# Performance work log

Hardware: AMD Instinct MI355X
Metric: run time of the kernel (lower is better)

## Reference

```python
import jax, jax.numpy as jnp
import numpy as np

B = 4096
STATE_DIM = 64
OBS_DIM = 32
BASE_DEGREE = 8
TIME_STEPS = 96
EPS = 1e-7


def _degree(t):
    # get_degree: degree_params initialized to linspace(0,1,time_steps); used via .item() (static)
    p = float(t) / (TIME_STEPS - 1)
    scaled = 0.5 * (1.0 + np.sin(2.0 * np.pi * p))
    return BASE_DEGREE + int(2.0 * scaled)


def _cheby_fwd_and_jac(x, coeffs, degree):
    """ChebyKAN forward y[b,o] = sum_{i,d} coeffs[i,o,d] * cos(d*acos(clip(tanh(x[b,i]))))
    plus its analytic per-sample Jacobian J[b,o,i] (replaces the torch autograd loop)."""
    t_raw = jnp.tanh(x)                                   # [B, D]
    t_val = jnp.clip(t_raw, -1.0 + EPS, 1.0 - EPS)
    theta = jnp.arccos(t_val)                             # [B, D]
    dvals = jnp.arange(degree + 1, dtype=x.dtype)         # [deg+1]
    ang = theta[..., None] * dvals                        # [B, D, deg+1]
    cheb = jnp.cos(ang)
    ac = coeffs[..., : degree + 1]                        # [D, D, deg+1]
    y = jnp.einsum('bid,iod->bo', cheb, ac)               # [B, D]
    # d cheb / d x = d*sin(d*theta) * (1 - tanh(x)^2) * mask / sqrt(1 - t_val^2)
    mask = ((t_raw > -1.0 + EPS) & (t_raw < 1.0 - EPS)).astype(x.dtype)
    dtheta_dx = -(1.0 - t_raw * t_raw) * mask / jnp.sqrt(1.0 - t_val * t_val)  # [B, D]
    dcheb_dx = -dvals * jnp.sin(ang) * dtheta_dx[..., None]                    # [B, D, deg+1]
    jac = jnp.einsum('bid,iod->boi', dcheb_dx, ac)        # [B, D, D] = dY_o/dx_i
    return y, jac


def setup_inputs() -> dict:
    key = jax.random.key(0)
    ks = jax.random.split(key, 5)
    obs = jax.random.normal(ks[0], (B, OBS_DIM), jnp.float32)
    prev_state = jax.random.normal(ks[1], (B, STATE_DIM), jnp.float32)
    A = jax.random.normal(ks[2], (B, STATE_DIM, STATE_DIM), jnp.float32)
    prev_cov = A @ A.transpose(0, 2, 1) / STATE_DIM + jnp.eye(STATE_DIM, dtype=jnp.float32)  # SPD
    bound = 1.0 / np.sqrt(STATE_DIM * (BASE_DEGREE + 3))  # kaiming-uniform style
    coeffs = jax.random.uniform(ks[3], (STATE_DIM, STATE_DIM, BASE_DEGREE + 3), jnp.float32, -bound, bound)
    M = jax.random.normal(ks[4], (STATE_DIM, OBS_DIM), jnp.float32)
    q, _ = jnp.linalg.qr(M)                               # orthonormal columns
    obs_matrix = q.T.astype(jnp.float32)                  # [OBS_DIM, STATE_DIM], orthogonal rows
    log_Q_diag = jnp.zeros((STATE_DIM,), jnp.float32)
    log_R_diag = jnp.zeros((OBS_DIM,), jnp.float32)
    return dict(obs=obs, prev_state=prev_state, prev_cov=prev_cov, coeffs=coeffs,
                obs_matrix=obs_matrix, log_Q_diag=log_Q_diag, log_R_diag=log_R_diag, t=10)


def reference(obs, prev_state, prev_cov, coeffs, obs_matrix, log_Q_diag, log_R_diag, t):
    degree = _degree(t)
    state_pred, Fj = _cheby_fwd_and_jac(prev_state, coeffs, degree)   # [B,D], [B,D,D]
    q = jnp.exp(log_Q_diag)                                           # [D]
    r = jnp.exp(log_R_diag)                                           # [O]
    H = obs_matrix                                                    # [O, D]
    # cov_pred = F P F^T + Q
    cov_pred = jnp.einsum('bij,bjk,blk->bil', Fj, prev_cov, Fj) + jnp.diag(q)[None]
    obs_pred = state_pred @ H.T                                       # [B, O]
    residual = obs - obs_pred                                         # [B, O]
    # S = H Pp H^T + R
    S = jnp.einsum('ij,bjk,lk->bil', H, cov_pred, H) + jnp.diag(r)[None]
    S_inv = jnp.linalg.pinv(S)                                        # [B, O, O]
    PHt = jnp.einsum('bij,oj->bio', cov_pred, H)                      # [B, D, O]
    K = jnp.einsum('bio,bop->bip', PHt, S_inv)                        # [B, D, O]
    state_update = state_pred + jnp.einsum('bio,bo->bi', K, residual)
    I_KH = jnp.eye(STATE_DIM, dtype=cov_pred.dtype)[None] - jnp.einsum('bio,oj->bij', K, H)
    # Joseph form: (I-KH) Pp (I-KH)^T + K R K^T
    cov_update = (jnp.einsum('bij,bjk,blk->bil', I_KH, cov_pred, I_KH)
                  + jnp.einsum('bio,o,bjo->bij', K, r, K))
    cov_diag = jnp.diagonal(cov_update, axis1=1, axis2=2)
    return state_update, cov_update, cov_diag
```

## Files before the change

### kernel.cpp

```cpp
#include <hip/hip_runtime.h>
#include <math.h>


typedef float f4 __attribute__((ext_vector_type(4)));
typedef float f32x4 __attribute__((ext_vector_type(4)));
typedef short b16x8 __attribute__((ext_vector_type(8)));
typedef short b16x4 __attribute__((ext_vector_type(4)));
typedef unsigned int u32;
typedef unsigned int u32x4 __attribute__((ext_vector_type(4)));
typedef unsigned short u16;

#define EPSC 1e-7f
#define MFMA(a, b, c) __builtin_amdgcn_mfma_f32_16x16x32_bf16(a, b, c, 0, 0, 0)
static constexpr size_t CU_OFF = 4096 * 64;
static constexpr size_t CD_OFF = CU_OFF + 4096ull * 4096;

__device__ __forceinline__ void split2(float x, short &h, short &l) {
  u32 u = __float_as_uint(x);
  h = (short)(u >> 16);
  float rem = x - __uint_as_float(u & 0xffff0000u);
  l = (short)(__float_as_uint(rem) >> 16);
}
__device__ __forceinline__ u32 packsplit(float x) {
  u32 u = __float_as_uint(x) & 0xffff0000u;
  float rem = x - __uint_as_float(u);
  return u | (__float_as_uint(rem) >> 16);
}
__device__ __forceinline__ float unpackf(u32 v) {
  return __uint_as_float(v & 0xffff0000u) + __uint_as_float(v << 16);
}
union U8 { u32x4 u; b16x8 s; };
__device__ __forceinline__ void unpack8(u32x4 q0, u32x4 q1, b16x8 &hi,
                                        b16x8 &lo) {
  U8 H, L;
  H.u[0] = __builtin_amdgcn_perm(q0[1], q0[0], 0x07060302u);
  H.u[1] = __builtin_amdgcn_perm(q0[3], q0[2], 0x07060302u);
  H.u[2] = __builtin_amdgcn_perm(q1[1], q1[0], 0x07060302u);
  H.u[3] = __builtin_amdgcn_perm(q1[3], q1[2], 0x07060302u);
  L.u[0] = __builtin_amdgcn_perm(q0[1], q0[0], 0x05040100u);
  L.u[1] = __builtin_amdgcn_perm(q0[3], q0[2], 0x05040100u);
  L.u[2] = __builtin_amdgcn_perm(q1[1], q1[0], 0x05040100u);
  L.u[3] = __builtin_amdgcn_perm(q1[3], q1[2], 0x05040100u);
  hi = H.s;
  lo = L.s;
}
__device__ __forceinline__ void split8v(f4 a, f4 b, b16x8 &hi, b16x8 &lo) {
#pragma unroll
  for (int j = 0; j < 4; ++j) {
    short hh, ll;
    split2(a[j], hh, ll); hi[j] = hh; lo[j] = ll;
    split2(b[j], hh, ll); hi[4 + j] = hh; lo[4 + j] = ll;
  }
}

__global__ __launch_bounds__(256) void prep_kernel(
    const float *__restrict__ Hm, const float *__restrict__ logQ,
    const float *__restrict__ logR, void *__restrict__ ws) {
  u16 *Hh = (u16 *)ws;
  u16 *Hl = (u16 *)ws + 2048;
  float *wq = (float *)((char *)ws + 8192);
  float *wr = wq + 64;
  const int tid = (int)threadIdx.x;
  f4 a = *(const f4 *)(Hm + tid * 8);
  f4 b = *(const f4 *)(Hm + tid * 8 + 4);
  b16x8 hi, lo;
  split8v(a, b, hi, lo);
  *(b16x8 *)(Hh + tid * 8) = hi;
  *(b16x8 *)(Hl + tid * 8) = lo;
  if (tid < 64) wq[tid] = expf(logQ[tid]);
  else if (tid < 96) wr[tid - 64] = expf(logR[tid - 64]);
}

__global__ __launch_bounds__(256, 4) void kalman_fused(
    const float *__restrict__ obs, const float *__restrict__ prev_state,
    const float *__restrict__ prev_cov, const float *__restrict__ coeffs,
    const float *__restrict__ Hm, const int *__restrict__ tptr,
    const void *__restrict__ ws, float *__restrict__ out) {
  __shared__ __align__(16) unsigned char pool[40704];
  u16 *sPh = (u16 *)(pool);
  u16 *sPl = (u16 *)(pool + 8192);
  u32 *sT = (u32 *)(pool);
  u32 *sPHt = (u32 *)(pool);
  u32 *sK = (u32 *)(pool + 8192);
  u16 *sFh = (u16 *)(pool + 16384);
  u16 *sFl = (u16 *)(pool + 24576);
  u32 *sCov = (u32 *)(pool + 16384);
  float *ypart = (float *)(pool + 32768);
  float *sS = (float *)(pool + 32768);
  float *sChT = (float *)(pool + 33792);
  float *sDcT = (float *)(pool + 36864);
  float *sy = (float *)(pool + 39936);
  float *sresid = (float *)(pool + 40192);
  float *sq = (float *)(pool + 40320);
  float *sr = (float *)(pool + 40576);

  const u16 *wHh = (const u16 *)ws;
  const u16 *wHl = (const u16 *)ws + 2048;
  const float *wq = (const float *)((const char *)ws + 8192);
  const float *wr = wq + 64;

  const int tid = (int)threadIdx.x;
  const int b = (int)blockIdx.x;
  const int w = tid >> 6;
  const int l = tid & 63;
  const int lr = l & 15;
  const int h = l >> 4;

  const int tval = tptr[0];
  const float ang = 6.28318530717958647f * ((float)tval / 95.0f);
  const int D = 9 + (int)(1.0f + sinf(ang));

  {
    const float *Pg = prev_cov + (size_t)b * 4096;
#pragma unroll
    for (int e = 0; e < 4; ++e) {
      const int idx = tid + 256 * e;
      f4 v = *(const f4 *)(Pg + 4 * idx);
      const int r = idx >> 4, c = (idx & 15) * 4;
      const int x = (r & 7) << 3;
      b16x4 h4, l4;
#pragma unroll
      for (int j = 0; j < 4; ++j) {
        short hh, ll;
        split2(v[j], hh, ll);
        h4[j] = hh; l4[j] = ll;
      }
      *(b16x4 *)(sPh + r * 64 + (c ^ x)) = h4;
      *(b16x4 *)(sPl + r * 64 + (c ^ x)) = l4;
    }
    if (tid < 64) {
      sq[tid] = wq[tid];
      const float xx = prev_state[b * 64 + tid];
      const float tr_ = tanhf(xx);
      const float tv = fminf(fmaxf(tr_, -1.0f + EPSC), 1.0f - EPSC);
      const float sn = sqrtf(fmaxf(1.0f - tv * tv, 0.0f));
      const float mask = (tr_ > -1.0f + EPSC && tr_ < 1.0f - EPSC) ? 1.0f : 0.0f;
      const float dth = -(1.0f - tr_ * tr_) * mask / sn;
      float *ct = sChT + tid * 12;
      float *dt = sDcT + tid * 12;
      ct[0] = 1.f; ct[1] = tv; ct[11] = 0.f;
      dt[0] = 0.f; dt[1] = -dth * sn; dt[11] = 0.f;
      float cm2 = 1.f, cm1 = tv, sm2 = 0.f, sm1 = sn;
      const float tv2 = 2.f * tv;
#pragma unroll
      for (int d = 2; d <= 10; ++d) {
        const float cc = fmaf(tv2, cm1, -cm2);
        const float ss = fmaf(tv2, sm1, -sm2);
        ct[d] = (d < D) ? cc : 0.f;
        dt[d] = (d < D) ? (-dth * (float)d * ss) : 0.f;
        cm2 = cm1; cm1 = cc; sm2 = sm1; sm1 = ss;
      }
    } else if (tid < 96) {
      sr[tid - 64] = wr[tid - 64];
    }
  }
  __syncthreads();

  {
    const int o = tid & 63, g = tid >> 6;
    float yacc = 0.f;
    float fr[16];
#pragma unroll
    for (int ii = 0; ii < 16; ++ii) {
      const int i = g * 16 + ii;
      const float *cp = coeffs + (size_t)(i * 64 + o) * 11;
      f4 q0 = *(const f4 *)(cp);
      f4 q1 = *(const f4 *)(cp + 4);
      f4 q2 = *(const f4 *)(cp + 7);
      const float *ct = sChT + i * 12;
      const float *dt = sDcT + i * 12;
      f4 c0 = *(const f4 *)(ct), c1 = *(const f4 *)(ct + 4),
         c2 = *(const f4 *)(ct + 8);
      f4 e0 = *(const f4 *)(dt), e1 = *(const f4 *)(dt + 4),
         e2 = *(const f4 *)(dt + 8);
      float yac = q0[0];
      yac = fmaf(q0[1], c0[1], yac);
      yac = fmaf(q0[2], c0[2], yac);
      yac = fmaf(q0[3], c0[3], yac);
      yac = fmaf(q1[0], c1[0], yac);
      yac = fmaf(q1[1], c1[1], yac);
      yac = fmaf(q1[2], c1[2], yac);
      yac = fmaf(q1[3], c1[3], yac);
      yac = fmaf(q2[1], c2[0], yac);
      yac = fmaf(q2[2], c2[1], yac);
      yac = fmaf(q2[3], c2[2], yac);
      float fra = q0[1] * e0[1];
      fra = fmaf(q0[2], e0[2], fra);
      fra = fmaf(q0[3], e0[3], fra);
      fra = fmaf(q1[0], e1[0], fra);
      fra = fmaf(q1[1], e1[1], fra);
      fra = fmaf(q1[2], e1[2], fra);
      fra = fmaf(q1[3], e1[3], fra);
      fra = fmaf(q2[1], e2[0], fra);
      fra = fmaf(q2[2], e2[1], fra);
      fra = fmaf(q2[3], e2[2], fra);
      yacc += yac;
      fr[ii] = fra;
    }
    b16x8 fh0, fh1, fl0, fl1;
#pragma unroll
    for (int j = 0; j < 8; ++j) {
      short hh, ll;
      split2(fr[j], hh, ll); fh0[j] = hh; fl0[j] = ll;
      split2(fr[8 + j], hh, ll); fh1[j] = hh; fl1[j] = ll;
    }
    const int x = (o & 7) << 3;
    *(b16x8 *)(sFh + o * 64 + ((g * 16) ^ x)) = fh0;
    *(b16x8 *)(sFh + o * 64 + ((g * 16 + 8) ^ x)) = fh1;
    *(b16x8 *)(sFl + o * 64 + ((g * 16) ^ x)) = fl0;
    *(b16x8 *)(sFl + o * 64 + ((g * 16 + 8) ^ x)) = fl1;
    ypart[g * 64 + o] = yacc;
  }
  __syncthreads();

  if (tid < 64) {
    sy[tid] = ypart[tid] + ypart[64 + tid] + ypart[128 + tid] +
              ypart[192 + tid];
  }
  __builtin_amdgcn_wave_barrier();
  if (tid < 32) {
    float racc = obs[b * 32 + tid];
    const float *Hr = Hm + tid * 64;
#pragma unroll
    for (int s = 0; s < 64; s += 4) {
      f4 hv = *(const f4 *)(Hr + s);
      racc -= hv[0] * sy[s] + hv[1] * sy[s + 1] + hv[2] * sy[s + 2] +
              hv[3] * sy[s + 3];
    }
    sresid[tid] = racc;
  }

  f32x4 accT[4] = {{0.f, 0.f, 0.f, 0.f}, {0.f, 0.f, 0.f, 0.f},
                   {0.f, 0.f, 0.f, 0.f}, {0.f, 0.f, 0.f, 0.f}};
  {
    const int m = 16 * w + lr;
    const int xA = (m & 7) << 3;
#pragma unroll
    for (int kc = 0; kc < 2; ++kc) {
      const int k = kc * 32 + h * 8;
      b16x8 Ah = *(const b16x8 *)(sFh + m * 64 + (k ^ xA));
      b16x8 Al = *(const b16x8 *)(sFl + m * 64 + (k ^ xA));
#pragma unroll
      for (int t = 0; t < 4; ++t) {
        const int n = t * 16 + lr;
        const int xB = (n & 7) << 3;
        b16x8 Bh = *(const b16x8 *)(sPh + n * 64 + (k ^ xB));
        b16x8 Bl = *(const b16x8 *)(sPl + n * 64 + (k ^ xB));
        accT[t] = MFMA(Ah, Bh, accT[t]);
        accT[t] = MFMA(Al, Bh, accT[t]);
        accT[t] = MFMA(Ah, Bl, accT[t]);
      }
    }
  }
  __syncthreads();
  {
    const int r0 = 16 * w + h * 4;
#pragma unroll
    for (int t = 0; t < 4; ++t)
#pragma unroll
      for (int j = 0; j < 4; ++j) {
        const int rr = r0 + j, cc = t * 16 + lr;
        sT[rr * 64 + (cc ^ ((rr & 7) << 2))] = packsplit(accT[t][j]);
      }
  }

  f32x4 accC[4] = {{0.f, 0.f, 0.f, 0.f}, {0.f, 0.f, 0.f, 0.f},
                   {0.f, 0.f, 0.f, 0.f}, {0.f, 0.f, 0.f, 0.f}};
  {
    const int m = 16 * w + lr;
    const int xA = (m & 7) << 2;
    const u32 *Tb = sT + m * 64;
#pragma unroll
    for (int kc = 0; kc < 2; ++kc) {
      const int k = kc * 32 + h * 8;
      u32x4 q0 = *(const u32x4 *)(Tb + (k ^ xA));
      u32x4 q1 = *(const u32x4 *)(Tb + ((k + 4) ^ xA));
      b16x8 Ah, Al;
      unpack8(q0, q1, Ah, Al);
#pragma unroll
      for (int t = 0; t < 4; ++t) {
        const int n = t * 16 + lr;
        const int xB = (n & 7) << 3;
        b16x8 Bh = *(const b16x8 *)(sFh + n * 64 + (k ^ xB));
        b16x8 Bl = *(const b16x8 *)(sFl + n * 64 + (k ^ xB));
        accC[t] = MFMA(Ah, Bh, accC[t]);
        accC[t] = MFMA(Al, Bh, accC[t]);
        accC[t] = MFMA(Ah, Bl, accC[t]);
      }
    }
  }
  __syncthreads();
  {
    const int r0 = 16 * w + h * 4;
#pragma unroll
    for (int t = 0; t < 4; ++t)
#pragma unroll
      for (int j = 0; j < 4; ++j) {
        const int rr = r0 + j, cc = t * 16 + lr;
        float v = accC[t][j];
        if (rr == cc) v += sq[rr];
        sCov[rr * 64 + (cc ^ ((rr & 7) << 2))] = packsplit(v);
      }
  }

  {
    f32x4 acc[2] = {{0.f, 0.f, 0.f, 0.f}, {0.f, 0.f, 0.f, 0.f}};
    const int m = 16 * w + lr;
    const int xA = (m & 7) << 2;
    const u32 *Cb = sCov + m * 64;
#pragma unroll
    for (int kc = 0; kc < 2; ++kc) {
      const int k = kc * 32 + h * 8;
      u32x4 q0 = *(const u32x4 *)(Cb + (k ^ xA));
      u32x4 q1 = *(const u32x4 *)(Cb + ((k + 4) ^ xA));
      b16x8 Ah, Al;
      unpack8(q0, q1, Ah, Al);
#pragma unroll
      for (int t = 0; t < 2; ++t) {
        const int n = t * 16 + lr;
        b16x8 Bh = *(const b16x8 *)(wHh + n * 64 + k);
        b16x8 Bl = *(const b16x8 *)(wHl + n * 64 + k);
        acc[t] = MFMA(Ah, Bh, acc[t]);
        acc[t] = MFMA(Al, Bh, acc[t]);
        acc[t] = MFMA(Ah, Bl, acc[t]);
      }
    }
    const int r0 = 16 * w + h * 4;
#pragma unroll
    for (int t = 0; t < 2; ++t)
#pragma unroll
      for (int j = 0; j < 4; ++j) {
        const int rr = r0 + j, cc = t * 16 + lr;
        sPHt[rr * 32 + (cc ^ ((rr & 7) << 2))] = packsplit(acc[t][j]);
      }
  }
  __syncthreads();

  {
    const int tr = w >> 1, tc = w & 1;
    f32x4 acc = {0.f, 0.f, 0.f, 0.f};
    const int m = tr * 16 + lr;
    const int n = tc * 16 + lr;
#pragma unroll
    for (int kc = 0; kc < 2; ++kc) {
      const int k = kc * 32 + h * 8;
      b16x8 Ah = *(const b16x8 *)(wHh + m * 64 + k);
      b16x8 Al = *(const b16x8 *)(wHl + m * 64 + k);
      u32x4 q0, q1;
#pragma unroll
      for (int j = 0; j < 4; ++j)
        q0[j] = sPHt[(k + j) * 32 + (n ^ (j << 2))];
#pragma unroll
      for (int j = 0; j < 4; ++j)
        q1[j] = sPHt[(k + 4 + j) * 32 + (n ^ ((4 + j) << 2))];
      b16x8 Bh, Bl;
      unpack8(q0, q1, Bh, Bl);
      acc = MFMA(Ah, Bh, acc);
      acc = MFMA(Al, Bh, acc);
      acc = MFMA(Ah, Bl, acc);
    }
    const int r0 = tr * 16 + h * 4;
#pragma unroll
    for (int j = 0; j < 4; ++j) {
      const int rr = r0 + j, cc = tc * 16 + lr;
      float v = acc[j];
      if (rr == cc) v += sr[rr];
      sS[rr * 36 + cc] = v;
    }
  }
  __syncthreads();

  if (w == 0) {
    const int mr = l >> 1, half = l & 1;
    float s0[16];
    const float *gbase = sS + mr * 36 + half * 16;
    {
      f4 v0 = *(const f4 *)(gbase + 0), v1 = *(const f4 *)(gbase + 4);
      f4 v2 = *(const f4 *)(gbase + 8), v3 = *(const f4 *)(gbase + 12);
#pragma unroll
      for (int j = 0; j < 4; ++j) {
        s0[j] = v0[j]; s0[4 + j] = v1[j]; s0[8 + j] = v2[j]; s0[12 + j] = v3[j];
      }
    }
#pragma unroll
    for (int p = 0; p < 32; ++p) {
      const int ph = p >> 4, pi = p & 15;
      float prow[16];
#pragma unroll
      for (int j = 0; j < 16; ++j) prow[j] = __shfl(s0[j], 2 * p + half, 64);
      const float dpp = __shfl(s0[pi], 2 * p + ph, 64);
      const float d = 1.0f / dpp;
      const float fv = __shfl(s0[pi], (l & 62) + ph, 64);
      if (mr == p) {
#pragma unroll
        for (int j = 0; j < 16; ++j) s0[j] = prow[j] * d;
        if (half == ph) s0[pi] = d;
      } else {
        const float fd = fv * d;
#pragma unroll
        for (int j = 0; j < 16; ++j) s0[j] = fmaf(-fd, prow[j], s0[j]);
        if (half == ph) s0[pi] = -fd;
      }
    }
    float *wbase = sS + mr * 36 + half * 16;
    f4 w0 = {s0[0], s0[1], s0[2], s0[3]};
    f4 w1 = {s0[4], s0[5], s0[6], s0[7]};
    f4 w2 = {s0[8], s0[9], s0[10], s0[11]};
    f4 w3 = {s0[12], s0[13], s0[14], s0[15]};
    *(f4 *)(wbase + 0) = w0;
    *(f4 *)(wbase + 4) = w1;
    *(f4 *)(wbase + 8) = w2;
    *(f4 *)(wbase + 12) = w3;
  }
  __syncthreads();

  {
    f32x4 acc[2] = {{0.f, 0.f, 0.f, 0.f}, {0.f, 0.f, 0.f, 0.f}};
    const int m = 16 * w + lr;
    const int xA = (m & 7) << 2;
    const int k = h * 8;
    u32x4 q0 = *(const u32x4 *)(sPHt + m * 32 + (k ^ xA));
    u32x4 q1 = *(const u32x4 *)(sPHt + m * 32 + ((k + 4) ^ xA));
    b16x8 Ah, Al;
    unpack8(q0, q1, Ah, Al);
#pragma unroll
    for (int t = 0; t < 2; ++t) {
      const int n = t * 16 + lr;
      f4 b0 = *(const f4 *)(sS + n * 36 + k);
      f4 b1 = *(const f4 *)(sS + n * 36 + k + 4);
      b16x8 Bh, Bl;
      split8v(b0, b1, Bh, Bl);
      acc[t] = MFMA(Ah, Bh, acc[t]);
      acc[t] = MFMA(Al, Bh, acc[t]);
      acc[t] = MFMA(Ah, Bl, acc[t]);
    }
    const int r0 = 16 * w + h * 4;
#pragma unroll
    for (int t = 0; t < 2; ++t)
#pragma unroll
      for (int j = 0; j < 4; ++j) {
        const int rr = r0 + j, cc = t * 16 + lr;
        sK[rr * 32 + (cc ^ ((rr & 7) << 2))] = packsplit(acc[t][j]);
      }
  }
  __syncthreads();

  if (tid < 64) {
    float su = sy[tid];
    const int x = (tid & 7) << 2;
    const u32 *Kb = sK + tid * 32;
#pragma unroll
    for (int c0 = 0; c0 < 32; c0 += 4) {
      u32x4 q = *(const u32x4 *)(Kb + (c0 ^ x));
#pragma unroll
      for (int j = 0; j < 4; ++j)
        su = fmaf(unpackf(q[j]), sresid[c0 + j], su);
    }
    out[b * 64 + tid] = su;
  }
  {
    const int m = 16 * w + lr;
    const int xA = (m & 7) << 2;
    const int k = h * 8;
    u32x4 q0 = *(const u32x4 *)(sK + m * 32 + (k ^ xA));
    u32x4 q1 = *(const u32x4 *)(sK + m * 32 + ((k + 4) ^ xA));
#pragma unroll
    for (int j = 0; j < 4; ++j) {
      q0[j] ^= 0x80008000u;
      q1[j] ^= 0x80008000u;
    }
    b16x8 Ah, Al;
    unpack8(q0, q1, Ah, Al);
    const int r0 = 16 * w + h * 4;
    float *outc = out + CU_OFF + (size_t)b * 4096;
#pragma unroll
    for (int t = 0; t < 4; ++t) {
      const int n = t * 16 + lr;
      const int xB = (n & 7) << 2;
      u32x4 p0 = *(const u32x4 *)(sPHt + n * 32 + (k ^ xB));
      u32x4 p1 = *(const u32x4 *)(sPHt + n * 32 + ((k + 4) ^ xB));
      b16x8 Bh, Bl;
      unpack8(p0, p1, Bh, Bl);
      f32x4 acc;
#pragma unroll
      for (int j = 0; j < 4; ++j) {
        const int rr = r0 + j;
        acc[j] = unpackf(sCov[rr * 64 + (n ^ ((rr & 7) << 2))]);
      }
      acc = MFMA(Ah, Bh, acc);
      acc = MFMA(Al, Bh, acc);
      acc = MFMA(Ah, Bl, acc);
#pragma unroll
      for (int j = 0; j < 4; ++j) {
        const int rr = r0 + j;
        outc[rr * 64 + n] = acc[j];
        if (rr == n) out[CD_OFF + b * 64 + rr] = acc[j];
      }
    }
  }
}

extern "C" void kernel_launch(void *const *d_in, const int *in_sizes, int n_in,
                              void *d_out, int out_size, void *d_ws,
                              size_t ws_size, hipStream_t stream) {
  const float *obs = (const float *)d_in[0];
  const float *prev_state = (const float *)d_in[1];
  const float *prev_cov = (const float *)d_in[2];
  const float *coeffs = (const float *)d_in[3];
  const float *Hm = (const float *)d_in[4];
  const float *logQ = (const float *)d_in[5];
  const float *logR = (const float *)d_in[6];
  const int *tptr = (const int *)d_in[7];
  (void)in_sizes; (void)n_in; (void)out_size; (void)ws_size;
  prep_kernel<<<dim3(1), dim3(256), 0, stream>>>(Hm, logQ, logR, d_ws);
  kalman_fused<<<dim3(4096), dim3(256), 0, stream>>>(
      obs, prev_state, prev_cov, coeffs, Hm, tptr, d_ws, (float *)d_out);
}
```

Baseline: 121.1 us.

## Shrink LDS pool, drop prep kernel, and defer cov split to raise occupancy

Removes the separate prep kernel and instead splits H into bf16 hi/lo and computes exp(logQ/logR) inline in the fused kernel. Shared memory drops from about 40 KB to 32 KB by aliasing the Chebyshev tables and partial sums into the covariance region, keeping y and the residual in registers passed by shuffles, and storing S in packed split form. To make the aliasing legal, prev_cov is loaded into registers early and split into LDS only after the Jacobian phase. Launch bounds rise to 5 blocks per CU. The cost is extra global loads and repeated split work for H in every block, plus an added barrier.

```diff
diff --git a/kernel.cpp b/kernel.cpp
--- a/kernel.cpp
+++ b/kernel.cpp
@@ -53,51 +53,25 @@
   }
 }
 
-__global__ __launch_bounds__(256) void prep_kernel(
-    const float *__restrict__ Hm, const float *__restrict__ logQ,
-    const float *__restrict__ logR, void *__restrict__ ws) {
-  u16 *Hh = (u16 *)ws;
-  u16 *Hl = (u16 *)ws + 2048;
-  float *wq = (float *)((char *)ws + 8192);
-  float *wr = wq + 64;
-  const int tid = (int)threadIdx.x;
-  f4 a = *(const f4 *)(Hm + tid * 8);
-  f4 b = *(const f4 *)(Hm + tid * 8 + 4);
-  b16x8 hi, lo;
-  split8v(a, b, hi, lo);
-  *(b16x8 *)(Hh + tid * 8) = hi;
-  *(b16x8 *)(Hl + tid * 8) = lo;
-  if (tid < 64) wq[tid] = expf(logQ[tid]);
-  else if (tid < 96) wr[tid - 64] = expf(logR[tid - 64]);
-}
-
-__global__ __launch_bounds__(256, 4) void kalman_fused(
+__global__ __launch_bounds__(256, 5) void kalman_fused(
     const float *__restrict__ obs, const float *__restrict__ prev_state,
     const float *__restrict__ prev_cov, const float *__restrict__ coeffs,
-    const float *__restrict__ Hm, const int *__restrict__ tptr,
-    const void *__restrict__ ws, float *__restrict__ out) {
-  __shared__ __align__(16) unsigned char pool[40704];
+    const float *__restrict__ Hm, const float *__restrict__ logQ,
+    const float *__restrict__ logR, const int *__restrict__ tptr,
+    float *__restrict__ out) {
+  __shared__ __align__(16) unsigned char pool[32768];
   u16 *sPh = (u16 *)(pool);
   u16 *sPl = (u16 *)(pool + 8192);
   u32 *sT = (u32 *)(pool);
   u32 *sPHt = (u32 *)(pool);
+  u32 *sSpk = (u32 *)(pool + 8192);
   u32 *sK = (u32 *)(pool + 8192);
   u16 *sFh = (u16 *)(pool + 16384);
   u16 *sFl = (u16 *)(pool + 24576);
   u32 *sCov = (u32 *)(pool + 16384);
-  float *ypart = (float *)(pool + 32768);
-  float *sS = (float *)(pool + 32768);
-  float *sChT = (float *)(pool + 33792);
-  float *sDcT = (float *)(pool + 36864);
-  float *sy = (float *)(pool + 39936);
-  float *sresid = (float *)(pool + 40192);
-  float *sq = (float *)(pool + 40320);
-  float *sr = (float *)(pool + 40576);
-
-  const u16 *wHh = (const u16 *)ws;
-  const u16 *wHl = (const u16 *)ws + 2048;
-  const float *wq = (const float *)((const char *)ws + 8192);
-  const float *wr = wq + 64;
+  float *sChT = (float *)(pool);
+  float *sDcT = (float *)(pool + 3072);
+  float *ypart = (float *)(pool + 6144);
 
   const int tid = (int)threadIdx.x;
   const int b = (int)blockIdx.x;
@@ -105,31 +79,18 @@
   const int l = tid & 63;
   const int lr = l & 15;
   const int h = l >> 4;
-
-  const int tval = tptr[0];
-  const float ang = 6.28318530717958647f * ((float)tval / 95.0f);
-  const int D = 9 + (int)(1.0f + sinf(ang));
-
+  const int rowbase = (w == 0) ? 48 : 16 * (w - 1);
+
+  f4 pr[4];
   {
     const float *Pg = prev_cov + (size_t)b * 4096;
 #pragma unroll
-    for (int e = 0; e < 4; ++e) {
-      const int idx = tid + 256 * e;
-      f4 v = *(const f4 *)(Pg + 4 * idx);
-      const int r = idx >> 4, c = (idx & 15) * 4;
-      const int x = (r & 7) << 3;
-      b16x4 h4, l4;
-#pragma unroll
-      for (int j = 0; j < 4; ++j) {
-        short hh, ll;
-        split2(v[j], hh, ll);
-        h4[j] = hh; l4[j] = ll;
-      }
-      *(b16x4 *)(sPh + r * 64 + (c ^ x)) = h4;
-      *(b16x4 *)(sPl + r * 64 + (c ^ x)) = l4;
-    }
+    for (int e = 0; e < 4; ++e)
+      pr[e] = *(const f4 *)(Pg + (rowbase + 4 * e + h) * 64 + lr * 4);
     if (tid < 64) {
-      sq[tid] = wq[tid];
+      const int tval = tptr[0];
+      const float ang = 6.28318530717958647f * ((float)tval / 95.0f);
+      const int D = 9 + (int)(1.0f + sinf(ang));
       const float xx = prev_state[b * 64 + tid];
       const float tr_ = tanhf(xx);
       const float tv = fminf(fmaxf(tr_, -1.0f + EPSC), 1.0f - EPSC);
@@ -150,8 +111,6 @@
         dt[d] = (d < D) ? (-dth * (float)d * ss) : 0.f;
         cm2 = cm1; cm1 = cc; sm2 = sm1; sm1 = ss;
       }
-    } else if (tid < 96) {
-      sr[tid - 64] = wr[tid - 64];
     }
   }
   __syncthreads();
@@ -213,22 +172,37 @@
   }
   __syncthreads();
 
-  if (tid < 64) {
-    sy[tid] = ypart[tid] + ypart[64 + tid] + ypart[128 + tid] +
-              ypart[192 + tid];
-  }
-  __builtin_amdgcn_wave_barrier();
-  if (tid < 32) {
-    float racc = obs[b * 32 + tid];
-    const float *Hr = Hm + tid * 64;
-#pragma unroll
-    for (int s = 0; s < 64; s += 4) {
-      f4 hv = *(const f4 *)(Hr + s);
-      racc -= hv[0] * sy[s] + hv[1] * sy[s + 1] + hv[2] * sy[s + 2] +
-              hv[3] * sy[s + 3];
-    }
-    sresid[tid] = racc;
-  }
+  float syl = 0.f, residreg = 0.f;
+  if (w == 0)
+    syl = ypart[l] + ypart[64 + l] + ypart[128 + l] + ypart[192 + l];
+#pragma unroll
+  for (int e = 0; e < 4; ++e) {
+    const int row = rowbase + 4 * e + h;
+    const int x = (row & 7) << 3;
+    b16x4 h4, l4;
+#pragma unroll
+    for (int j = 0; j < 4; ++j) {
+      short hh, ll;
+      split2(pr[e][j], hh, ll);
+      h4[j] = hh; l4[j] = ll;
+    }
+    *(b16x4 *)(sPh + row * 64 + ((lr * 4) ^ x)) = h4;
+    *(b16x4 *)(sPl + row * 64 + ((lr * 4) ^ x)) = l4;
+  }
+  if (w == 0) {
+    const int r = l & 31;
+    float racc = obs[b * 32 + r];
+    const float *Hr = Hm + r * 64;
+#pragma unroll
+    for (int c = 0; c < 64; c += 4) {
+      f4 hv = *(const f4 *)(Hr + c);
+#pragma unroll
+      for (int j = 0; j < 4; ++j)
+        racc = fmaf(-hv[j], __shfl(syl, c + j, 64), racc);
+    }
+    residreg = racc;
+  }
+  __syncthreads();
 
   f32x4 accT[4] = {{0.f, 0.f, 0.f, 0.f}, {0.f, 0.f, 0.f, 0.f},
                    {0.f, 0.f, 0.f, 0.f}, {0.f, 0.f, 0.f, 0.f}};
@@ -292,13 +266,17 @@
   __syncthreads();
   {
     const int r0 = 16 * w + h * 4;
+    f4 lq = *(const f4 *)(logQ + r0);
+    float qv[4];
+#pragma unroll
+    for (int j = 0; j < 4; ++j) qv[j] = expf(lq[j]);
 #pragma unroll
     for (int t = 0; t < 4; ++t)
 #pragma unroll
       for (int j = 0; j < 4; ++j) {
         const int rr = r0 + j, cc = t * 16 + lr;
         float v = accC[t][j];
-        if (rr == cc) v += sq[rr];
+        if (rr == cc) v += qv[j];
         sCov[rr * 64 + (cc ^ ((rr & 7) << 2))] = packsplit(v);
       }
   }
@@ -318,8 +296,11 @@
 #pragma unroll
       for (int t = 0; t < 2; ++t) {
         const int n = t * 16 + lr;
-        b16x8 Bh = *(const b16x8 *)(wHh + n * 64 + k);
-        b16x8 Bl = *(const b16x8 *)(wHl + n * 64 + k);
+        const float *Hr = Hm + n * 64 + k;
+        f4 b0 = *(const f4 *)(Hr);
+        f4 b1 = *(const f4 *)(Hr + 4);
+        b16x8 Bh, Bl;
+        split8v(b0, b1, Bh, Bl);
         acc[t] = MFMA(Ah, Bh, acc[t]);
         acc[t] = MFMA(Al, Bh, acc[t]);
         acc[t] = MFMA(Ah, Bl, acc[t]);
@@ -344,8 +325,11 @@
 #pragma unroll
     for (int kc = 0; kc < 2; ++kc) {
       const int k = kc * 32 + h * 8;
-      b16x8 Ah = *(const b16x8 *)(wHh + m * 64 + k);
-      b16x8 Al = *(const b16x8 *)(wHl + m * 64 + k);
+      const float *Hr = Hm + m * 64 + k;
+      f4 a0 = *(const f4 *)(Hr);
+      f4 a1 = *(const f4 *)(Hr + 4);
+      b16x8 Ah, Al;
+      split8v(a0, a1, Ah, Al);
       u32x4 q0, q1;
 #pragma unroll
       for (int j = 0; j < 4; ++j)
@@ -359,28 +343,27 @@
       acc = MFMA(Al, Bh, acc);
       acc = MFMA(Ah, Bl, acc);
     }
-    const int r0 = tr * 16 + h * 4;
+    const int r0s = tr * 16 + h * 4;
+    f4 lrv = *(const f4 *)(logR + r0s);
 #pragma unroll
     for (int j = 0; j < 4; ++j) {
-      const int rr = r0 + j, cc = tc * 16 + lr;
+      const int rr = r0s + j, cc = tc * 16 + lr;
       float v = acc[j];
-      if (rr == cc) v += sr[rr];
-      sS[rr * 36 + cc] = v;
+      if (rr == cc) v += expf(lrv[j]);
+      sSpk[rr * 32 + (cc ^ ((rr & 7) << 2))] = packsplit(v);
     }
   }
   __syncthreads();
 
   if (w == 0) {
     const int mr = l >> 1, half = l & 1;
+    const int xm = (mr & 7) << 2;
     float s0[16];
-    const float *gbase = sS + mr * 36 + half * 16;
-    {
-      f4 v0 = *(const f4 *)(gbase + 0), v1 = *(const f4 *)(gbase + 4);
-      f4 v2 = *(const f4 *)(gbase + 8), v3 = *(const f4 *)(gbase + 12);
-#pragma unroll
-      for (int j = 0; j < 4; ++j) {
-        s0[j] = v0[j]; s0[4 + j] = v1[j]; s0[8 + j] = v2[j]; s0[12 + j] = v3[j];
-      }
+#pragma unroll
+    for (int qi = 0; qi < 4; ++qi) {
+      u32x4 qv = *(const u32x4 *)(sSpk + mr * 32 + ((half * 16 + qi * 4) ^ xm));
+#pragma unroll
+      for (int j = 0; j < 4; ++j) s0[qi * 4 + j] = unpackf(qv[j]);
     }
 #pragma unroll
     for (int p = 0; p < 32; ++p) {
@@ -402,20 +385,18 @@
         if (half == ph) s0[pi] = -fd;
       }
     }
-    float *wbase = sS + mr * 36 + half * 16;
-    f4 w0 = {s0[0], s0[1], s0[2], s0[3]};
-    f4 w1 = {s0[4], s0[5], s0[6], s0[7]};
-    f4 w2 = {s0[8], s0[9], s0[10], s0[11]};
-    f4 w3 = {s0[12], s0[13], s0[14], s0[15]};
-    *(f4 *)(wbase + 0) = w0;
-    *(f4 *)(wbase + 4) = w1;
-    *(f4 *)(wbase + 8) = w2;
-    *(f4 *)(wbase + 12) = w3;
-  }
-  __syncthreads();
-
-  {
-    f32x4 acc[2] = {{0.f, 0.f, 0.f, 0.f}, {0.f, 0.f, 0.f, 0.f}};
+#pragma unroll
+    for (int qi = 0; qi < 4; ++qi) {
+      u32x4 ov;
+#pragma unroll
+      for (int j = 0; j < 4; ++j) ov[j] = packsplit(s0[qi * 4 + j]);
+      *(u32x4 *)(sSpk + mr * 32 + ((half * 16 + qi * 4) ^ xm)) = ov;
+    }
+  }
+  __syncthreads();
+
+  f32x4 accK[2] = {{0.f, 0.f, 0.f, 0.f}, {0.f, 0.f, 0.f, 0.f}};
+  {
     const int m = 16 * w + lr;
     const int xA = (m & 7) << 2;
     const int k = h * 8;
@@ -426,37 +407,41 @@
 #pragma unroll
     for (int t = 0; t < 2; ++t) {
       const int n = t * 16 + lr;
-      f4 b0 = *(const f4 *)(sS + n * 36 + k);
-      f4 b1 = *(const f4 *)(sS + n * 36 + k + 4);
+      const int xB = (n & 7) << 2;
+      u32x4 b0 = *(const u32x4 *)(sSpk + n * 32 + (k ^ xB));
+      u32x4 b1 = *(const u32x4 *)(sSpk + n * 32 + ((k + 4) ^ xB));
       b16x8 Bh, Bl;
-      split8v(b0, b1, Bh, Bl);
-      acc[t] = MFMA(Ah, Bh, acc[t]);
-      acc[t] = MFMA(Al, Bh, acc[t]);
-      acc[t] = MFMA(Ah, Bl, acc[t]);
-    }
+      unpack8(b0, b1, Bh, Bl);
+      accK[t] = MFMA(Ah, Bh, accK[t]);
+      accK[t] = MFMA(Al, Bh, accK[t]);
+      accK[t] = MFMA(Ah, Bl, accK[t]);
+    }
+  }
+  __syncthreads();
+  {
     const int r0 = 16 * w + h * 4;
 #pragma unroll
     for (int t = 0; t < 2; ++t)
 #pragma unroll
       for (int j = 0; j < 4; ++j) {
         const int rr = r0 + j, cc = t * 16 + lr;
-        sK[rr * 32 + (cc ^ ((rr & 7) << 2))] = packsplit(acc[t][j]);
+        sK[rr * 32 + (cc ^ ((rr & 7) << 2))] = packsplit(accK[t][j]);
       }
   }
   __syncthreads();
 
   if (tid < 64) {
-    float su = sy[tid];
-    const int x = (tid & 7) << 2;
-    const u32 *Kb = sK + tid * 32;
+    float su = syl;
+    const int x = (l & 7) << 2;
+    const u32 *Kb = sK + l * 32;
 #pragma unroll
     for (int c0 = 0; c0 < 32; c0 += 4) {
       u32x4 q = *(const u32x4 *)(Kb + (c0 ^ x));
 #pragma unroll
       for (int j = 0; j < 4; ++j)
-        su = fmaf(unpackf(q[j]), sresid[c0 + j], su);
-    }
-    out[b * 64 + tid] = su;
+        su = fmaf(unpackf(q[j]), __shfl(residreg, c0 + j, 64), su);
+    }
+    out[b * 64 + l] = su;
   }
   {
     const int m = 16 * w + lr;
@@ -511,8 +496,7 @@
   const float *logQ = (const float *)d_in[5];
   const float *logR = (const float *)d_in[6];
   const int *tptr = (const int *)d_in[7];
-  (void)in_sizes; (void)n_in; (void)out_size; (void)ws_size;
-  prep_kernel<<<dim3(1), dim3(256), 0, stream>>>(Hm, logQ, logR, d_ws);
+  (void)in_sizes; (void)n_in; (void)out_size; (void)d_ws; (void)ws_size;
   kalman_fused<<<dim3(4096), dim3(256), 0, stream>>>(
-      obs, prev_state, prev_cov, coeffs, Hm, tptr, d_ws, (float *)d_out);
-}
+      obs, prev_state, prev_cov, coeffs, Hm, logQ, logR, tptr, (float *)d_out);
+}
```

New measurement: 171.6 us. 41.7% more time.
